# Performance work log

Measured on AMD Instinct MI355X. Metric: run time of the kernel, lower is better.

## Reference

```python
import jax, jax.numpy as jnp
import numpy as np

B, S, D, H = 4, 2048, 1024, 16
DEPTH = D // H
NEG = -1e9


def setup_inputs() -> dict:
    key = jax.random.key(0)
    ks = jax.random.split(key, 10)
    scale = 1.0 / np.sqrt(D)
    return {
        "query": jax.random.normal(ks[0], (B, S, D), jnp.float32),
        "key": jax.random.normal(ks[1], (B, S, D), jnp.float32),
        "value": jax.random.normal(ks[2], (B, S, D), jnp.float32),
        "mask": jnp.zeros((B, 1, 1, S), jnp.float32),
        "Wq": jax.random.normal(ks[3], (D, D), jnp.float32) * scale,
        "bq": jnp.zeros((D,), jnp.float32),
        "Wk": jax.random.normal(ks[4], (D, D), jnp.float32) * scale,
        "bk": jnp.zeros((D,), jnp.float32),
        "Wv": jax.random.normal(ks[5], (D, D), jnp.float32) * scale,
        "bv": jnp.zeros((D,), jnp.float32),
        "Wo": jax.random.normal(ks[6], (D, D), jnp.float32) * scale,
        "bo": jnp.zeros((D,), jnp.float32),
    }


def _split_heads(x):
    # [B, S, D] -> [B, H, S, depth]
    b, s, _ = x.shape
    return x.reshape(b, s, H, DEPTH).transpose(0, 2, 1, 3)


def reference(query, key, value, mask, Wq, bq, Wk, bk, Wv, bv, Wo, bo):
    q = _split_heads(query @ Wq + bq)
    k = _split_heads(key @ Wk + bk)
    v = _split_heads(value @ Wv + bv)
    # scaled dot-product attention
    logits = jnp.einsum("bhqd,bhkd->bhqk", q, k) / jnp.sqrt(
        jnp.asarray(DEPTH, jnp.float32))
    logits = logits + mask * NEG
    attn = jax.nn.softmax(logits, axis=-1)
    out = jnp.einsum("bhqk,bhkd->bhqd", attn, v)
    # merge heads: [B,H,S,depth] -> [B,S,D]
    out = out.transpose(0, 2, 1, 3).reshape(query.shape[0], -1, D)
    out = out @ Wo + bo
    return out, attn
```

## Files before the change

kernel.cpp:

```cpp
#include <hip/hip_runtime.h>
#include <stdint.h>


typedef float f32x4 __attribute__((ext_vector_type(4)));
typedef __bf16 bf16x8 __attribute__((ext_vector_type(8)));
typedef unsigned short u16x4 __attribute__((ext_vector_type(4)));

#define LOG2E 1.44269504088896340736f

static __device__ __forceinline__ f32x4 mfma16(bf16x8 a, bf16x8 b, f32x4 c) {
  return __builtin_amdgcn_mfma_f32_16x16x32_bf16(a, b, c, 0, 0, 0);
}
static __device__ __forceinline__ unsigned short bfc(float f) {
  return __builtin_bit_cast(unsigned short, (__bf16)f);
}
static __device__ __forceinline__ float e2(float x) { return __builtin_amdgcn_exp2f(x); }

#define GLDS16(g, l)                                                    \
  __builtin_amdgcn_global_load_lds(                                     \
      (const __attribute__((address_space(1))) void*)(g),               \
      (__attribute__((address_space(3))) void*)(l), 16, 0, 0)

__global__ void cvt_bf16(const float* __restrict__ x, unsigned short* __restrict__ y) {
  const int i = (blockIdx.x * 256 + threadIdx.x) * 4;
  f32x4 v = *(const f32x4*)(const void*)(x + i);
  u16x4 o;
  o[0] = bfc(v[0]); o[1] = bfc(v[1]); o[2] = bfc(v[2]); o[3] = bfc(v[3]);
  *(u16x4*)(void*)(y + i) = o;
}

__global__ void wtrans(const float* __restrict__ W, unsigned short* __restrict__ Wt) {
  __shared__ float t[32][33];
  const int tx = threadIdx.x & 31, ty = threadIdx.x >> 5;
  const int n0 = blockIdx.x * 32, k0 = blockIdx.y * 32;
#pragma unroll
  for (int i = 0; i < 4; ++i)
    t[ty + i * 8][tx] = W[(size_t)(k0 + ty + i * 8) * 1024 + n0 + tx];
  __syncthreads();
#pragma unroll
  for (int i = 0; i < 4; ++i)
    Wt[(size_t)(n0 + ty + i * 8) * 1024 + k0 + tx] = bfc(t[tx][ty + i * 8]);
}

template <int E>
__global__ __launch_bounds__(256, 2) void gemm_bt(const unsigned short* __restrict__ A,
                                                  const unsigned short* __restrict__ Bt,
                                                  const float* __restrict__ bias,
                                                  void* __restrict__ Cout) {
  __shared__ unsigned short sA[128 * 32];
  __shared__ unsigned short sB[128 * 32];
  const int tid = threadIdx.x;
  const int m0 = blockIdx.x << 7, n0 = blockIdx.y << 7;
  const int w = tid >> 6, lane = tid & 63, g = lane >> 4, r = lane & 15;
  const int wr = w >> 1, wc = w & 1;
  const f32x4 fz = {0.f, 0.f, 0.f, 0.f};
  f32x4 acc[4][4];
#pragma unroll
  for (int i = 0; i < 4; ++i)
#pragma unroll
    for (int j = 0; j < 4; ++j) acc[i][j] = fz;

  const int srow = tid >> 2;
  const int scol = (tid & 3) << 3;
  const unsigned short* ga = A + (size_t)(m0 + srow) * 1024 + scol;
  const unsigned short* gb = Bt + (size_t)(n0 + srow) * 1024 + scol;
  unsigned short* la = sA + tid * 8;
  unsigned short* lb = sB + tid * 8;

  for (int kt = 0; kt < 32; ++kt) {
    const int ko = kt << 5;
    GLDS16(ga + ko, la);
    GLDS16(ga + ko + 64 * 1024, la + 64 * 32);
    GLDS16(gb + ko, lb);
    GLDS16(gb + ko + 64 * 1024, lb + 64 * 32);
    __syncthreads();
    bf16x8 af[4], bfv[4];
#pragma unroll
    for (int i = 0; i < 4; ++i) {
      af[i]  = *(const bf16x8*)(const void*)&sA[(wr * 64 + i * 16 + r) * 32 + g * 8];
      bfv[i] = *(const bf16x8*)(const void*)&sB[(wc * 64 + i * 16 + r) * 32 + g * 8];
    }
#pragma unroll
    for (int i = 0; i < 4; ++i)
#pragma unroll
      for (int j = 0; j < 4; ++j) acc[i][j] = mfma16(af[i], bfv[j], acc[i][j]);
    __syncthreads();
  }

  float bv[4];
#pragma unroll
  for (int j = 0; j < 4; ++j) bv[j] = bias[n0 + wc * 64 + j * 16 + r];
#pragma unroll
  for (int i = 0; i < 4; ++i) {
#pragma unroll
    for (int j = 0; j < 4; ++j) {
#pragma unroll
      for (int t = 0; t < 4; ++t) {
        const float c = acc[i][j][t] + bv[j];
        const int m = m0 + wr * 64 + i * 16 + g * 4 + t;
        const int n = n0 + wc * 64 + j * 16 + r;
        if (E == 2) {
          ((float*)Cout)[(size_t)m * 1024 + n] = c;
        } else {
          const int bb = m >> 11, s = m & 2047, hh = n >> 6, d = n & 63;
          if (E == 0)
            ((unsigned short*)Cout)[(size_t)(bb * 16 + hh) * 131072 + (size_t)s * 64 + d] = bfc(c);
          else
            ((unsigned short*)Cout)[(size_t)(bb * 16 + hh) * 131072 + (size_t)d * 2048 + s] = bfc(c);
        }
      }
    }
  }
}

__global__ __launch_bounds__(256, 2) void attn_fused(const unsigned short* __restrict__ Qh,
                                                     const unsigned short* __restrict__ Kh,
                                                     const unsigned short* __restrict__ Vt,
                                                     const float* __restrict__ mask,
                                                     float* __restrict__ attn_out,
                                                     unsigned short* __restrict__ Obuf) {
  __shared__ unsigned short Plds[4][64 * 40];
  __shared__ float Osum[64][68];
  __shared__ float sml[4][64];

  const int blk = (blockIdx.x & 7) * 256 + (blockIdx.x >> 3);
  const int bh = blk >> 5;
  const int q0 = (blk & 31) << 6;
  const int b = bh >> 4, h = bh & 15;
  const int tid = threadIdx.x;
  const int w = tid >> 6, lane = tid & 63, g = lane >> 4, r = lane & 15;
  const float SCL = 0.125f * LOG2E;
  const float NEGM = -1e9f * LOG2E;

  const unsigned short* Qb = Qh + (size_t)bh * (2048 * 64);
  const unsigned short* Kb = Kh + (size_t)bh * (2048 * 64);
  const unsigned short* Vb = Vt + (size_t)bh * (64 * 2048);
  const float* mb = mask + (size_t)b * 2048;
  const f32x4 fz = {0.f, 0.f, 0.f, 0.f};

  bf16x8 qf[4][2];
#pragma unroll
  for (int qc = 0; qc < 4; ++qc)
#pragma unroll
    for (int hf = 0; hf < 2; ++hf)
      qf[qc][hf] = *(const bf16x8*)(const void*)(Qb + (size_t)(q0 + qc * 16 + r) * 64 + hf * 32 + g * 8);

  float lreg[4] = {0.f, 0.f, 0.f, 0.f};

  for (int step = 0; step < 16; ++step) {
    const int kk = (w << 9) + (step << 5);
    bf16x8 kf[2][2];
#pragma unroll
    for (int ks = 0; ks < 2; ++ks)
#pragma unroll
      for (int hf = 0; hf < 2; ++hf)
        kf[ks][hf] = *(const bf16x8*)(const void*)(Kb + (size_t)(kk + ks * 16 + r) * 64 + hf * 32 + g * 8);
    f32x4 mp[2];
#pragma unroll
    for (int ks = 0; ks < 2; ++ks) {
      f32x4 mv = *(const f32x4*)(const void*)(mb + kk + ks * 16 + g * 4);
#pragma unroll
      for (int j = 0; j < 4; ++j) mp[ks][j] = mv[j] * NEGM;
    }

#pragma unroll
    for (int qc = 0; qc < 4; ++qc) {
      f32x4 s0 = fz, s1 = fz;
      s0 = mfma16(kf[0][0], qf[qc][0], s0);
      s0 = mfma16(kf[0][1], qf[qc][1], s0);
      s1 = mfma16(kf[1][0], qf[qc][0], s1);
      s1 = mfma16(kf[1][1], qf[qc][1], s1);
      float p = 0.f;
#pragma unroll
      for (int j = 0; j < 4; ++j) {
        p += e2(fmaf(s0[j], SCL, mp[0][j]));
        p += e2(fmaf(s1[j], SCL, mp[1][j]));
      }
      lreg[qc] += p;
    }
  }
#pragma unroll
  for (int qc = 0; qc < 4; ++qc) {
    lreg[qc] += __shfl_xor(lreg[qc], 16);
    lreg[qc] += __shfl_xor(lreg[qc], 32);
  }
  if (lane < 16) {
#pragma unroll
    for (int qc = 0; qc < 4; ++qc) sml[w][qc * 16 + lane] = lreg[qc];
  }
  __syncthreads();
  float invL[4];
#pragma unroll
  for (int qc = 0; qc < 4; ++qc) {
    const int q = qc * 16 + r;
    invL[qc] = 1.f / (sml[0][q] + sml[1][q] + sml[2][q] + sml[3][q]);
  }

  f32x4 oacc[4][4];
#pragma unroll
  for (int i = 0; i < 4; ++i)
#pragma unroll
    for (int j = 0; j < 4; ++j) oacc[i][j] = fz;

  float* ab = attn_out + (size_t)bh * 2048 * 2048;

  for (int step = 0; step < 16; ++step) {
    const int kk = (w << 9) + (step << 5);
    bf16x8 kf[2][2];
#pragma unroll
    for (int ks = 0; ks < 2; ++ks)
#pragma unroll
      for (int hf = 0; hf < 2; ++hf)
        kf[ks][hf] = *(const bf16x8*)(const void*)(Kb + (size_t)(kk + ks * 16 + r) * 64 + hf * 32 + g * 8);
    f32x4 mp[2];
#pragma unroll
    for (int ks = 0; ks < 2; ++ks) {
      f32x4 mv = *(const f32x4*)(const void*)(mb + kk + ks * 16 + g * 4);
#pragma unroll
      for (int j = 0; j < 4; ++j) mp[ks][j] = mv[j] * NEGM;
    }

#pragma unroll
    for (int ks = 0; ks < 2; ++ks) {
#pragma unroll
      for (int qc = 0; qc < 4; ++qc) {
        f32x4 s = fz;
        s = mfma16(kf[ks][0], qf[qc][0], s);
        s = mfma16(kf[ks][1], qf[qc][1], s);
        f32x4 pv;
        u16x4 pb;
#pragma unroll
        for (int j = 0; j < 4; ++j) {
          const float val = e2(fmaf(s[j], SCL, mp[ks][j])) * invL[qc];
          pv[j] = val;
          pb[j] = bfc(val);
        }
        __builtin_nontemporal_store(
            pv, (f32x4*)(void*)(ab + (size_t)(q0 + qc * 16 + r) * 2048 + kk + ks * 16 + g * 4));
        *(u16x4*)(void*)(&Plds[w][(qc * 16 + r) * 40 + ks * 16 + g * 4]) = pb;
      }
    }
    bf16x8 vf[4];
#pragma unroll
    for (int dn = 0; dn < 4; ++dn)
      vf[dn] = *(const bf16x8*)(const void*)(Vb + (size_t)(dn * 16 + r) * 2048 + kk + g * 8);
#pragma unroll
    for (int qs = 0; qs < 4; ++qs) {
      const bf16x8 pa = *(const bf16x8*)(const void*)(&Plds[w][(qs * 16 + r) * 40 + g * 8]);
#pragma unroll
      for (int dn = 0; dn < 4; ++dn) oacc[qs][dn] = mfma16(pa, vf[dn], oacc[qs][dn]);
    }
  }

  for (int wv = 0; wv < 4; ++wv) {
    if (w == wv) {
#pragma unroll
      for (int qs = 0; qs < 4; ++qs)
#pragma unroll
        for (int dn = 0; dn < 4; ++dn)
#pragma unroll
          for (int j = 0; j < 4; ++j) {
            const int q = qs * 16 + g * 4 + j, d = dn * 16 + r;
            if (wv == 0) Osum[q][d] = oacc[qs][dn][j];
            else         Osum[q][d] += oacc[qs][dn][j];
          }
    }
    __syncthreads();
  }
  const int orow = tid >> 2, oc0 = (tid & 3) << 4;
#pragma unroll
  for (int i = 0; i < 4; ++i) {
    u16x4 pk;
#pragma unroll
    for (int j = 0; j < 4; ++j) pk[j] = bfc(Osum[orow][oc0 + i * 4 + j]);
    *(u16x4*)(void*)(Obuf + (size_t)(b * 2048 + q0 + orow) * 1024 + h * 64 + oc0 + i * 4) = pk;
  }
}

extern "C" void kernel_launch(void* const* d_in, const int* in_sizes, int n_in,
                              void* d_out, int out_size, void* d_ws, size_t ws_size,
                              hipStream_t stream) {
  const float* query = (const float*)d_in[0];
  const float* key_  = (const float*)d_in[1];
  const float* value = (const float*)d_in[2];
  const float* mask  = (const float*)d_in[3];
  const float* Wq = (const float*)d_in[4];
  const float* bq = (const float*)d_in[5];
  const float* Wk = (const float*)d_in[6];
  const float* bk = (const float*)d_in[7];
  const float* Wv = (const float*)d_in[8];
  const float* bv = (const float*)d_in[9];
  const float* Wo = (const float*)d_in[10];
  const float* bo = (const float*)d_in[11];

  uint8_t* ws = (uint8_t*)d_ws;
  unsigned short* XQ  = (unsigned short*)(ws);
  unsigned short* XK  = (unsigned short*)(ws + 16777216);
  unsigned short* XV  = (unsigned short*)(ws + 33554432);
  unsigned short* WTQ = (unsigned short*)(ws + 50331648);
  unsigned short* WTK = (unsigned short*)(ws + 52428800);
  unsigned short* WTV = (unsigned short*)(ws + 54525952);
  unsigned short* WTO = (unsigned short*)(ws + 56623104);
  unsigned short* QH  = (unsigned short*)(ws + 58720256);
  unsigned short* KH  = (unsigned short*)(ws + 75497472);
  unsigned short* VT  = (unsigned short*)(ws + 92274688);
  unsigned short* OB  = XQ;

  float* outp = (float*)d_out;
  float* attnp = outp + 8388608;

  cvt_bf16<<<8192, 256, 0, stream>>>(query, XQ);
  cvt_bf16<<<8192, 256, 0, stream>>>(key_, XK);
  cvt_bf16<<<8192, 256, 0, stream>>>(value, XV);
  wtrans<<<dim3(32, 32), 256, 0, stream>>>(Wq, WTQ);
  wtrans<<<dim3(32, 32), 256, 0, stream>>>(Wk, WTK);
  wtrans<<<dim3(32, 32), 256, 0, stream>>>(Wv, WTV);
  wtrans<<<dim3(32, 32), 256, 0, stream>>>(Wo, WTO);
  gemm_bt<0><<<dim3(64, 8), 256, 0, stream>>>(XQ, WTQ, bq, QH);
  gemm_bt<0><<<dim3(64, 8), 256, 0, stream>>>(XK, WTK, bk, KH);
  gemm_bt<1><<<dim3(64, 8), 256, 0, stream>>>(XV, WTV, bv, VT);
  attn_fused<<<2048, 256, 0, stream>>>(QH, KH, VT, mask, attnp, OB);
  gemm_bt<2><<<dim3(64, 8), 256, 0, stream>>>(OB, WTO, bo, outp);
}
```

Before: 486.5 us.

## Batch launches, vectorize GEMM epilogues, fold softmax scale into Q projection

Merges the three input conversions, four weight transposes and the Q/K projections into single launches indexed by blockIdx.z. The GEMM epilogues swap MFMA operand order so each lane holds contiguous columns, which allows vector bias loads and 4-wide stores. The attention scale is folded into the Q projection, and the mask add is skipped when a tile's mask bits are all zero. The normalisation multiply becomes a log-sum subtraction inside exp2. The mask test adds a branch, and pre-scaling Q before bf16 rounding slightly changes numerics.

```diff
diff --git a/kernel.cpp b/kernel.cpp
--- a/kernel.cpp
+++ b/kernel.cpp
@@ -5,6 +5,7 @@
 typedef float f32x4 __attribute__((ext_vector_type(4)));
 typedef __bf16 bf16x8 __attribute__((ext_vector_type(8)));
 typedef unsigned short u16x4 __attribute__((ext_vector_type(4)));
+typedef unsigned short u16x8 __attribute__((ext_vector_type(8)));
 
 #define LOG2E 1.44269504088896340736f
 
@@ -21,16 +22,29 @@
       (const __attribute__((address_space(1))) void*)(g),               \
       (__attribute__((address_space(3))) void*)(l), 16, 0, 0)
 
-__global__ void cvt_bf16(const float* __restrict__ x, unsigned short* __restrict__ y) {
+struct Ptr3 { const float* s[3]; unsigned short* d[3]; };
+struct Ptr4 { const float* s[4]; unsigned short* d[4]; };
+struct QKArgs {
+  const unsigned short* A[2];
+  const unsigned short* Bt[2];
+  const float* bias[2];
+  unsigned short* C[2];
+};
+
+__global__ void cvt3(Ptr3 p) {
+  const int z = blockIdx.z;
   const int i = (blockIdx.x * 256 + threadIdx.x) * 4;
-  f32x4 v = *(const f32x4*)(const void*)(x + i);
+  f32x4 v = *(const f32x4*)(const void*)(p.s[z] + i);
   u16x4 o;
   o[0] = bfc(v[0]); o[1] = bfc(v[1]); o[2] = bfc(v[2]); o[3] = bfc(v[3]);
-  *(u16x4*)(void*)(y + i) = o;
-}
-
-__global__ void wtrans(const float* __restrict__ W, unsigned short* __restrict__ Wt) {
+  *(u16x4*)(void*)(p.d[z] + i) = o;
+}
+
+__global__ void wtrans4(Ptr4 p) {
   __shared__ float t[32][33];
+  const int z = blockIdx.z;
+  const float* W = p.s[z];
+  unsigned short* Wt = p.d[z];
   const int tx = threadIdx.x & 31, ty = threadIdx.x >> 5;
   const int n0 = blockIdx.x * 32, k0 = blockIdx.y * 32;
 #pragma unroll
@@ -42,73 +56,124 @@
     Wt[(size_t)(n0 + ty + i * 8) * 1024 + k0 + tx] = bfc(t[tx][ty + i * 8]);
 }
 
-template <int E>
-__global__ __launch_bounds__(256, 2) void gemm_bt(const unsigned short* __restrict__ A,
-                                                  const unsigned short* __restrict__ Bt,
-                                                  const float* __restrict__ bias,
-                                                  void* __restrict__ Cout) {
-  __shared__ unsigned short sA[128 * 32];
-  __shared__ unsigned short sB[128 * 32];
-  const int tid = threadIdx.x;
-  const int m0 = blockIdx.x << 7, n0 = blockIdx.y << 7;
-  const int w = tid >> 6, lane = tid & 63, g = lane >> 4, r = lane & 15;
-  const int wr = w >> 1, wc = w & 1;
+#define GEMM_PROLOG(Aptr, Btptr)                                        \
+  __shared__ unsigned short sA[128 * 32];                               \
+  __shared__ unsigned short sB[128 * 32];                               \
+  const int tid = threadIdx.x;                                          \
+  const int m0 = blockIdx.x << 7, n0 = blockIdx.y << 7;                 \
+  const int w = tid >> 6, lane = tid & 63, g = lane >> 4, r = lane & 15;\
+  const int wr = w >> 1, wc = w & 1;                                    \
+  const int srow = tid >> 2;                                            \
+  const int scol = (tid & 3) << 3;                                      \
+  const unsigned short* ga = (Aptr) + (size_t)(m0 + srow) * 1024 + scol;\
+  const unsigned short* gb = (Btptr) + (size_t)(n0 + srow) * 1024 + scol;\
+  unsigned short* la = sA + tid * 8;                                    \
+  unsigned short* lb = sB + tid * 8;
+
+#define GEMM_KLOOP(SWAP)                                                \
+  for (int kt = 0; kt < 32; ++kt) {                                     \
+    const int ko = kt << 5;                                             \
+    GLDS16(ga + ko, la);                                                \
+    GLDS16(ga + ko + 64 * 1024, la + 64 * 32);                          \
+    GLDS16(gb + ko, lb);                                                \
+    GLDS16(gb + ko + 64 * 1024, lb + 64 * 32);                          \
+    __syncthreads();                                                    \
+    bf16x8 af[4], bfv[4];                                               \
+    _Pragma("unroll")                                                   \
+    for (int i = 0; i < 4; ++i) {                                       \
+      af[i]  = *(const bf16x8*)(const void*)&sA[(wr * 64 + i * 16 + r) * 32 + g * 8]; \
+      bfv[i] = *(const bf16x8*)(const void*)&sB[(wc * 64 + i * 16 + r) * 32 + g * 8]; \
+    }                                                                   \
+    _Pragma("unroll")                                                   \
+    for (int i = 0; i < 4; ++i)                                         \
+      _Pragma("unroll")                                                 \
+      for (int j = 0; j < 4; ++j)                                       \
+        acc[i][j] = (SWAP) ? mfma16(bfv[j], af[i], acc[i][j])           \
+                           : mfma16(af[i], bfv[j], acc[i][j]);          \
+    __syncthreads();                                                    \
+  }
+
+__global__ __launch_bounds__(256, 2) void gemm_qk(QKArgs args) {
+  const int z = blockIdx.z;
   const f32x4 fz = {0.f, 0.f, 0.f, 0.f};
   f32x4 acc[4][4];
 #pragma unroll
   for (int i = 0; i < 4; ++i)
 #pragma unroll
     for (int j = 0; j < 4; ++j) acc[i][j] = fz;
-
-  const int srow = tid >> 2;
-  const int scol = (tid & 3) << 3;
-  const unsigned short* ga = A + (size_t)(m0 + srow) * 1024 + scol;
-  const unsigned short* gb = Bt + (size_t)(n0 + srow) * 1024 + scol;
-  unsigned short* la = sA + tid * 8;
-  unsigned short* lb = sB + tid * 8;
-
-  for (int kt = 0; kt < 32; ++kt) {
-    const int ko = kt << 5;
-    GLDS16(ga + ko, la);
-    GLDS16(ga + ko + 64 * 1024, la + 64 * 32);
-    GLDS16(gb + ko, lb);
-    GLDS16(gb + ko + 64 * 1024, lb + 64 * 32);
-    __syncthreads();
-    bf16x8 af[4], bfv[4];
+  GEMM_PROLOG(args.A[z], args.Bt[z])
+  GEMM_KLOOP(1)
+  const float osc = (z == 0) ? (0.125f * LOG2E) : 1.0f;
+  unsigned short* Cq = args.C[z];
+  const float* bias = args.bias[z];
+#pragma unroll
+  for (int j = 0; j < 4; ++j) {
+    const int nb = n0 + wc * 64 + j * 16 + g * 4;
+    const f32x4 b4 = *(const f32x4*)(const void*)(bias + nb);
 #pragma unroll
     for (int i = 0; i < 4; ++i) {
-      af[i]  = *(const bf16x8*)(const void*)&sA[(wr * 64 + i * 16 + r) * 32 + g * 8];
-      bfv[i] = *(const bf16x8*)(const void*)&sB[(wc * 64 + i * 16 + r) * 32 + g * 8];
-    }
-#pragma unroll
-    for (int i = 0; i < 4; ++i)
-#pragma unroll
-      for (int j = 0; j < 4; ++j) acc[i][j] = mfma16(af[i], bfv[j], acc[i][j]);
-    __syncthreads();
-  }
-
-  float bv[4];
-#pragma unroll
-  for (int j = 0; j < 4; ++j) bv[j] = bias[n0 + wc * 64 + j * 16 + r];
-#pragma unroll
-  for (int i = 0; i < 4; ++i) {
-#pragma unroll
-    for (int j = 0; j < 4; ++j) {
-#pragma unroll
-      for (int t = 0; t < 4; ++t) {
-        const float c = acc[i][j][t] + bv[j];
-        const int m = m0 + wr * 64 + i * 16 + g * 4 + t;
-        const int n = n0 + wc * 64 + j * 16 + r;
-        if (E == 2) {
-          ((float*)Cout)[(size_t)m * 1024 + n] = c;
-        } else {
-          const int bb = m >> 11, s = m & 2047, hh = n >> 6, d = n & 63;
-          if (E == 0)
-            ((unsigned short*)Cout)[(size_t)(bb * 16 + hh) * 131072 + (size_t)s * 64 + d] = bfc(c);
-          else
-            ((unsigned short*)Cout)[(size_t)(bb * 16 + hh) * 131072 + (size_t)d * 2048 + s] = bfc(c);
-        }
-      }
+      const int m = m0 + wr * 64 + i * 16 + r;
+      const int bb = m >> 11, s = m & 2047, hh = nb >> 6, d = nb & 63;
+      u16x4 pk;
+#pragma unroll
+      for (int t = 0; t < 4; ++t) pk[t] = bfc((acc[i][j][t] + b4[t]) * osc);
+      *(u16x4*)(void*)(Cq + (size_t)(bb * 16 + hh) * 131072 + (size_t)s * 64 + d) = pk;
+    }
+  }
+}
+
+__global__ __launch_bounds__(256, 2) void gemm_v(const unsigned short* __restrict__ A,
+                                                 const unsigned short* __restrict__ Bt,
+                                                 const float* __restrict__ bias,
+                                                 unsigned short* __restrict__ C) {
+  const f32x4 fz = {0.f, 0.f, 0.f, 0.f};
+  f32x4 acc[4][4];
+#pragma unroll
+  for (int i = 0; i < 4; ++i)
+#pragma unroll
+    for (int j = 0; j < 4; ++j) acc[i][j] = fz;
+  GEMM_PROLOG(A, Bt)
+  GEMM_KLOOP(0)
+#pragma unroll
+  for (int j = 0; j < 4; ++j) {
+    const int n = n0 + wc * 64 + j * 16 + r;
+    const float bv = bias[n];
+    const int hh = n >> 6, d = n & 63;
+#pragma unroll
+    for (int i = 0; i < 4; ++i) {
+      const int m = m0 + wr * 64 + i * 16 + g * 4;
+      const int bb = m >> 11, s = m & 2047;
+      u16x4 pk;
+#pragma unroll
+      for (int t = 0; t < 4; ++t) pk[t] = bfc(acc[i][j][t] + bv);
+      *(u16x4*)(void*)(C + (size_t)(bb * 16 + hh) * 131072 + (size_t)d * 2048 + s) = pk;
+    }
+  }
+}
+
+__global__ __launch_bounds__(256, 2) void gemm_o(const unsigned short* __restrict__ A,
+                                                 const unsigned short* __restrict__ Bt,
+                                                 const float* __restrict__ bias,
+                                                 float* __restrict__ C) {
+  const f32x4 fz = {0.f, 0.f, 0.f, 0.f};
+  f32x4 acc[4][4];
+#pragma unroll
+  for (int i = 0; i < 4; ++i)
+#pragma unroll
+    for (int j = 0; j < 4; ++j) acc[i][j] = fz;
+  GEMM_PROLOG(A, Bt)
+  GEMM_KLOOP(1)
+#pragma unroll
+  for (int j = 0; j < 4; ++j) {
+    const int nb = n0 + wc * 64 + j * 16 + g * 4;
+    const f32x4 b4 = *(const f32x4*)(const void*)(bias + nb);
+#pragma unroll
+    for (int i = 0; i < 4; ++i) {
+      const int m = m0 + wr * 64 + i * 16 + r;
+      f32x4 c;
+#pragma unroll
+      for (int t = 0; t < 4; ++t) c[t] = acc[i][j][t] + b4[t];
+      *(f32x4*)(void*)(C + (size_t)m * 1024 + nb) = c;
     }
   }
 }
@@ -129,7 +194,6 @@
   const int b = bh >> 4, h = bh & 15;
   const int tid = threadIdx.x;
   const int w = tid >> 6, lane = tid & 63, g = lane >> 4, r = lane & 15;
-  const float SCL = 0.125f * LOG2E;
   const float NEGM = -1e9f * LOG2E;
 
   const unsigned short* Qb = Qh + (size_t)bh * (2048 * 64);
@@ -155,28 +219,41 @@
 #pragma unroll
       for (int hf = 0; hf < 2; ++hf)
         kf[ks][hf] = *(const bf16x8*)(const void*)(Kb + (size_t)(kk + ks * 16 + r) * 64 + hf * 32 + g * 8);
-    f32x4 mp[2];
-#pragma unroll
-    for (int ks = 0; ks < 2; ++ks) {
-      f32x4 mv = *(const f32x4*)(const void*)(mb + kk + ks * 16 + g * 4);
-#pragma unroll
-      for (int j = 0; j < 4; ++j) mp[ks][j] = mv[j] * NEGM;
-    }
-
+    f32x4 mv0 = *(const f32x4*)(const void*)(mb + kk + g * 4);
+    f32x4 mv1 = *(const f32x4*)(const void*)(mb + kk + 16 + g * 4);
+    unsigned int mbits = 0;
+#pragma unroll
+    for (int j = 0; j < 4; ++j)
+      mbits |= __builtin_bit_cast(unsigned int, mv0[j]) | __builtin_bit_cast(unsigned int, mv1[j]);
+
+    f32x4 s0[4], s1[4];
 #pragma unroll
     for (int qc = 0; qc < 4; ++qc) {
-      f32x4 s0 = fz, s1 = fz;
-      s0 = mfma16(kf[0][0], qf[qc][0], s0);
-      s0 = mfma16(kf[0][1], qf[qc][1], s0);
-      s1 = mfma16(kf[1][0], qf[qc][0], s1);
-      s1 = mfma16(kf[1][1], qf[qc][1], s1);
-      float p = 0.f;
-#pragma unroll
-      for (int j = 0; j < 4; ++j) {
-        p += e2(fmaf(s0[j], SCL, mp[0][j]));
-        p += e2(fmaf(s1[j], SCL, mp[1][j]));
+      s0[qc] = fz; s1[qc] = fz;
+      s0[qc] = mfma16(kf[0][0], qf[qc][0], s0[qc]);
+      s0[qc] = mfma16(kf[0][1], qf[qc][1], s0[qc]);
+      s1[qc] = mfma16(kf[1][0], qf[qc][0], s1[qc]);
+      s1[qc] = mfma16(kf[1][1], qf[qc][1], s1[qc]);
+    }
+    if (__builtin_expect(mbits == 0, 1)) {
+#pragma unroll
+      for (int qc = 0; qc < 4; ++qc) {
+        float p = 0.f;
+#pragma unroll
+        for (int j = 0; j < 4; ++j) p += e2(s0[qc][j]) + e2(s1[qc][j]);
+        lreg[qc] += p;
       }
-      lreg[qc] += p;
+    } else {
+      f32x4 mp0, mp1;
+#pragma unroll
+      for (int j = 0; j < 4; ++j) { mp0[j] = mv0[j] * NEGM; mp1[j] = mv1[j] * NEGM; }
+#pragma unroll
+      for (int qc = 0; qc < 4; ++qc) {
+        float p = 0.f;
+#pragma unroll
+        for (int j = 0; j < 4; ++j) p += e2(s0[qc][j] + mp0[j]) + e2(s1[qc][j] + mp1[j]);
+        lreg[qc] += p;
+      }
     }
   }
 #pragma unroll
@@ -189,11 +266,13 @@
     for (int qc = 0; qc < 4; ++qc) sml[w][qc * 16 + lane] = lreg[qc];
   }
   __syncthreads();
-  float invL[4];
+  float cL[4], invL[4];
 #pragma unroll
   for (int qc = 0; qc < 4; ++qc) {
     const int q = qc * 16 + r;
-    invL[qc] = 1.f / (sml[0][q] + sml[1][q] + sml[2][q] + sml[3][q]);
+    const float L = sml[0][q] + sml[1][q] + sml[2][q] + sml[3][q];
+    cL[qc] = -__log2f(L);
+    invL[qc] = 1.f / L;
   }
 
   f32x4 oacc[4][4];
@@ -212,12 +291,21 @@
 #pragma unroll
       for (int hf = 0; hf < 2; ++hf)
         kf[ks][hf] = *(const bf16x8*)(const void*)(Kb + (size_t)(kk + ks * 16 + r) * 64 + hf * 32 + g * 8);
+    f32x4 mv0 = *(const f32x4*)(const void*)(mb + kk + g * 4);
+    f32x4 mv1 = *(const f32x4*)(const void*)(mb + kk + 16 + g * 4);
+    unsigned int mbits = 0;
+#pragma unroll
+    for (int j = 0; j < 4; ++j)
+      mbits |= __builtin_bit_cast(unsigned int, mv0[j]) | __builtin_bit_cast(unsigned int, mv1[j]);
     f32x4 mp[2];
-#pragma unroll
-    for (int ks = 0; ks < 2; ++ks) {
-      f32x4 mv = *(const f32x4*)(const void*)(mb + kk + ks * 16 + g * 4);
-#pragma unroll
-      for (int j = 0; j < 4; ++j) mp[ks][j] = mv[j] * NEGM;
+    if (__builtin_expect(mbits != 0, 0)) {
+#pragma unroll
+      for (int j = 0; j < 4; ++j) {
+        mp[0][j] = mv0[j] * NEGM;
+        mp[1][j] = mv1[j] * NEGM;
+      }
+    } else {
+      mp[0] = fz; mp[1] = fz;
     }
 
 #pragma unroll
@@ -231,7 +319,7 @@
         u16x4 pb;
 #pragma unroll
         for (int j = 0; j < 4; ++j) {
-          const float val = e2(fmaf(s[j], SCL, mp[ks][j])) * invL[qc];
+          const float val = e2(s[j] + mp[ks][j] + cL[qc]);
           pv[j] = val;
           pb[j] = bfc(val);
         }
@@ -267,13 +355,14 @@
     }
     __syncthreads();
   }
+  (void)invL;
   const int orow = tid >> 2, oc0 = (tid & 3) << 4;
 #pragma unroll
-  for (int i = 0; i < 4; ++i) {
-    u16x4 pk;
-#pragma unroll
-    for (int j = 0; j < 4; ++j) pk[j] = bfc(Osum[orow][oc0 + i * 4 + j]);
-    *(u16x4*)(void*)(Obuf + (size_t)(b * 2048 + q0 + orow) * 1024 + h * 64 + oc0 + i * 4) = pk;
+  for (int half = 0; half < 2; ++half) {
+    u16x8 pk;
+#pragma unroll
+    for (int j = 0; j < 8; ++j) pk[j] = bfc(Osum[orow][oc0 + half * 8 + j]);
+    *(u16x8*)(void*)(Obuf + (size_t)(b * 2048 + q0 + orow) * 1024 + h * 64 + oc0 + half * 8) = pk;
   }
 }
 
@@ -309,16 +398,13 @@
   float* outp = (float*)d_out;
   float* attnp = outp + 8388608;
 
-  cvt_bf16<<<8192, 256, 0, stream>>>(query, XQ);
-  cvt_bf16<<<8192, 256, 0, stream>>>(key_, XK);
-  cvt_bf16<<<8192, 256, 0, stream>>>(value, XV);
-  wtrans<<<dim3(32, 32), 256, 0, stream>>>(Wq, WTQ);
-  wtrans<<<dim3(32, 32), 256, 0, stream>>>(Wk, WTK);
-  wtrans<<<dim3(32, 32), 256, 0, stream>>>(Wv, WTV);
-  wtrans<<<dim3(32, 32), 256, 0, stream>>>(Wo, WTO);
-  gemm_bt<0><<<dim3(64, 8), 256, 0, stream>>>(XQ, WTQ, bq, QH);
-  gemm_bt<0><<<dim3(64, 8), 256, 0, stream>>>(XK, WTK, bk, KH);
-  gemm_bt<1><<<dim3(64, 8), 256, 0, stream>>>(XV, WTV, bv, VT);
+  Ptr3 pc = {{query, key_, value}, {XQ, XK, XV}};
+  cvt3<<<dim3(8192, 1, 3), 256, 0, stream>>>(pc);
+  Ptr4 pw = {{Wq, Wk, Wv, Wo}, {WTQ, WTK, WTV, WTO}};
+  wtrans4<<<dim3(32, 32, 4), 256, 0, stream>>>(pw);
+  QKArgs qk = {{XQ, XK}, {WTQ, WTK}, {bq, bk}, {QH, KH}};
+  gemm_qk<<<dim3(64, 8, 2), 256, 0, stream>>>(qk);
+  gemm_v<<<dim3(64, 8), 256, 0, stream>>>(XV, WTV, bv, VT);
   attn_fused<<<2048, 256, 0, stream>>>(QH, KH, VT, mask, attnp, OB);
-  gemm_bt<2><<<dim3(64, 8), 256, 0, stream>>>(OB, WTO, bo, outp);
-}
+  gemm_o<<<dim3(64, 8), 256, 0, stream>>>(OB, WTO, bo, outp);
+}
```

New measurement: 498.0 us. 2.4% more time.
